# Performance work log

Measured on AMD Instinct MI355X. Metric: run time of the kernel, lower is better.

The kernel has to match this reference:

```python
import jax, jax.numpy as jnp
import numpy as np
from jax import lax

LN_EPS = 1e-5          # F.layer_norm default eps
W_EPS = 1e-7           # eps in ste_weights
Q_EPS = 1e-5           # BitLinear.eps used in activation clamp
Q_RANGE = 128          # 2**(num_bits-1), num_bits=8
DIM_IN = 2048
DIM_OUT = 8192
N_TOKENS = 8192


def setup_inputs() -> dict:
    key = jax.random.key(0)
    k1, k2 = jax.random.split(key)
    x = jax.random.normal(k1, (N_TOKENS, DIM_IN), dtype=jnp.float32)
    # nn.Linear default init: U(-1/sqrt(fan_in), 1/sqrt(fan_in))
    bound = 1.0 / np.sqrt(DIM_IN)
    weight = jax.random.uniform(k2, (DIM_OUT, DIM_IN), dtype=jnp.float32,
                                minval=-bound, maxval=bound)
    return {"x": x, "weight": weight}


def _bitlinear(x, weight):
    # layer_norm over feature dim, no affine params
    mu = jnp.mean(x, axis=-1, keepdims=True)
    var = jnp.mean(jnp.square(x - mu), axis=-1, keepdims=True)
    normed = (x - mu) * lax.rsqrt(var + LN_EPS)

    # scalars come from .item() in torch -> detached constants
    input_gamma = lax.stop_gradient(jnp.max(jnp.abs(normed)))
    w_gamma = lax.stop_gradient(jnp.mean(jnp.abs(weight)))

    # ternarize weights with straight-through estimator
    w_bin_ng = jnp.clip(jnp.round(weight / (w_gamma + W_EPS)), -1.0, 1.0)
    w_bin = weight + lax.stop_gradient(w_bin_ng - weight)

    # quantize activations to int8 range (kept in float, as in the source)
    q_in = jnp.clip(normed * (Q_RANGE / input_gamma),
                    -Q_RANGE + Q_EPS, Q_RANGE - Q_EPS)

    out = q_in @ w_bin.T  # [N, dim_out]; bias=False since mult_bias=False
    return out * (input_gamma * w_gamma / Q_RANGE)


def reference(x, weight):
    proj = _bitlinear(x, weight)               # [N, DIM_OUT]
    h, gate = jnp.split(proj, 2, axis=-1)      # chunk(2, dim=-1)
    return h * jax.nn.silu(gate)               # mult_bias == 1.0
```

## Files before the change

kernel.cpp:

```cpp
#include <hip/hip_runtime.h>
#include <hip/hip_bf16.h>
#include <cstdint>


#define N_TOK   8192
#define DIMIN   2048
#define DIMOUT  8192
#define NOUT    4096
#define W_ELEMS 16777216.0f
#define NPART   1024

typedef _Float16 f16x8 __attribute__((ext_vector_type(8)));
typedef _Float16 f16x4 __attribute__((ext_vector_type(4)));
typedef float    f32x4 __attribute__((ext_vector_type(4)));

__global__ __launch_bounds__(256) void ln_wsum_k(
    const float* __restrict__ x, const float* __restrict__ w,
    _Float16* __restrict__ qA, float* __restrict__ wpart) {
    const int b = blockIdx.x;
    const int t = threadIdx.x;
    if (b < N_TOK) {
        __shared__ float sh[8];
        const float4* xr = (const float4*)(x + (size_t)b * DIMIN);
        float4 a = xr[2 * t];
        float4 c = xr[2 * t + 1];
        float s = (a.x + a.y) + (a.z + a.w) + ((c.x + c.y) + (c.z + c.w));
#pragma unroll
        for (int o = 32; o > 0; o >>= 1) s += __shfl_down(s, o, 64);
        if ((t & 63) == 0) sh[t >> 6] = s;
        __syncthreads();
        const float mu = (sh[0] + sh[1] + sh[2] + sh[3]) * (1.0f / DIMIN);

        float d0 = a.x - mu, d1 = a.y - mu, d2 = a.z - mu, d3 = a.w - mu;
        float d4 = c.x - mu, d5 = c.y - mu, d6 = c.z - mu, d7 = c.w - mu;
        float ss = d0*d0 + d1*d1 + d2*d2 + d3*d3 + d4*d4 + d5*d5 + d6*d6 + d7*d7;
#pragma unroll
        for (int o = 32; o > 0; o >>= 1) ss += __shfl_down(ss, o, 64);
        if ((t & 63) == 0) sh[4 + (t >> 6)] = ss;
        __syncthreads();
        const float var = (sh[4] + sh[5] + sh[6] + sh[7]) * (1.0f / DIMIN);
        const float r = rsqrtf(var + 1e-5f);
        f16x8 o;
        o[0] = (_Float16)(d0 * r); o[1] = (_Float16)(d1 * r);
        o[2] = (_Float16)(d2 * r); o[3] = (_Float16)(d3 * r);
        o[4] = (_Float16)(d4 * r); o[5] = (_Float16)(d5 * r);
        o[6] = (_Float16)(d6 * r); o[7] = (_Float16)(d7 * r);
        ((f16x8*)(qA + (size_t)b * DIMIN))[t] = o;
    } else {
        const int p = b - N_TOK;
        float acc = 0.0f;
        const float4* w4 = (const float4*)w;
        for (unsigned i = (unsigned)p * 256u + t; i < 4194304u; i += 262144u) {
            float4 v = w4[i];
            acc += (fabsf(v.x) + fabsf(v.y)) + (fabsf(v.z) + fabsf(v.w));
        }
        __shared__ float shw[4];
#pragma unroll
        for (int o = 32; o > 0; o >>= 1) acc += __shfl_down(acc, o, 64);
        if ((t & 63) == 0) shw[t >> 6] = acc;
        __syncthreads();
        if (t == 0) wpart[p] = (shw[0] + shw[1]) + (shw[2] + shw[3]);
    }
}

__global__ __launch_bounds__(256) void ternW_k(
    const float* __restrict__ w, const float* __restrict__ wpart,
    float* __restrict__ sc, _Float16* __restrict__ q) {
    const int t = threadIdx.x;
    __shared__ float sh[4];
    float4 p = ((const float4*)wpart)[t];
    float acc = (p.x + p.y) + (p.z + p.w);
#pragma unroll
    for (int o = 32; o > 0; o >>= 1) acc += __shfl_down(acc, o, 64);
    if ((t & 63) == 0) sh[t >> 6] = acc;
    __syncthreads();
    const float wg = ((sh[0] + sh[1]) + (sh[2] + sh[3])) * (1.0f / W_ELEMS);
    if (blockIdx.x == 0 && t == 0) sc[0] = wg;
    const float invw = 1.0f / (wg + 1e-7f);
    for (unsigned i = blockIdx.x * 256u + t; i < 4194304u; i += 262144u) {
        float4 v = ((const float4*)w)[i];
        f16x4 o;
        o.x = (_Float16)fminf(fmaxf(rintf(v.x * invw), -1.0f), 1.0f);
        o.y = (_Float16)fminf(fmaxf(rintf(v.y * invw), -1.0f), 1.0f);
        o.z = (_Float16)fminf(fmaxf(rintf(v.z * invw), -1.0f), 1.0f);
        o.w = (_Float16)fminf(fmaxf(rintf(v.w * invw), -1.0f), 1.0f);
        ((f16x4*)q)[i] = o;
    }
}

__device__ __forceinline__ void ld16(const _Float16* g, _Float16* l) {
    __builtin_amdgcn_global_load_lds(
        (const __attribute__((address_space(1))) unsigned int*)g,
        (__attribute__((address_space(3))) unsigned int*)l, 16, 0, 0);
}


#define BAR    __builtin_amdgcn_s_barrier()
#define LGKM0  asm volatile("s_waitcnt lgkmcnt(0)" ::: "memory")
#define VMC(n) asm volatile("s_waitcnt vmcnt(" #n ")" ::: "memory")
#define PRIO1  __builtin_amdgcn_s_setprio(1)
#define PRIO0  __builtin_amdgcn_s_setprio(0)

#define MFMA16(ACC)                                                       \
    _Pragma("unroll") for (int mi = 0; mi < 4; ++mi)                      \
    _Pragma("unroll") for (int ni = 0; ni < 4; ++ni)                      \
        ACC[mi][ni] = __builtin_amdgcn_mfma_f32_16x16x32_f16(             \
            a[mi], b[ni], ACC[mi][ni], 0, 0, 0);

#define DS_AB(AOFF, BOFF_)                                                \
    _Pragma("unroll") for (int i = 0; i < 4; ++i) {                       \
        a[i] = *(const f16x8*)(Ac + (AOFF) + (i << 10));                  \
        b[i] = *(const f16x8*)(Bc + (BOFF_) + (i << 10));                 \
    }

#define DS_B(BOFF_)                                                       \
    _Pragma("unroll") for (int i = 0; i < 4; ++i)                         \
        b[i] = *(const f16x8*)(Bc + (BOFF_) + (i << 10));

__global__ __launch_bounds__(512, 2) void gemm_glu_k(
    const _Float16* __restrict__ Aq, const _Float16* __restrict__ Wq,
    const float* __restrict__ sc, float* __restrict__ out) {

    __shared__ __align__(16) _Float16 sm[65536];

    const int tid  = threadIdx.x;
    const int wave = tid >> 6;
    const int lane = tid & 63;

    const int swz = ((blockIdx.x & 7) << 7) + (blockIdx.x >> 3);
    const int m0 = (swz >> 5) << 8;
    const int n0 = (swz & 31) << 7;

    const int rs = (wave << 3) + (lane >> 3);
    const int kc = (((lane & 7) ^ ((lane >> 3) & 7)) << 3);
    const _Float16* pa = Aq + (size_t)(m0 + rs) * DIMIN + kc;
    const _Float16* pb = Wq + (size_t)(n0 + rs) * DIMIN + kc;

    const int fr   = lane & 15;
    const int quad = lane >> 4;
    const int xr   = fr & 7;
    const int wm = (wave >> 1) << 6;
    const int wn = (wave & 1) << 6;
    const int a0off = (wm + fr) * 64 + ((quad ^ xr) << 3);
    const int a1off = (wm + fr) * 64 + (((quad + 4) ^ xr) << 3);
    const int b0off = (wn + fr) * 64 + ((quad ^ xr) << 3);
    const int b1off = (wn + fr) * 64 + (((quad + 4) ^ xr) << 3);

    const float s = sc[0];

    f32x4 z = {0.0f, 0.0f, 0.0f, 0.0f};
    f32x4 acc_h[4][4], acc_g[4][4];
#pragma unroll
    for (int i = 0; i < 4; ++i)
#pragma unroll
        for (int j = 0; j < 4; ++j) { acc_h[i][j] = z; acc_g[i][j] = z; }

    {
        _Float16* dA = sm + (wave << 9);
        _Float16* dB = dA + 32768;
        ld16(pb,           dB);
        ld16(pb + 131072,  dB + 4096);
        ld16(pa,           dA);
        ld16(pa + 131072,  dA + 4096);
        ld16(pa + 262144,  dA + 8192);
        ld16(pa + 393216,  dA + 12288);
        ld16(pb + 8388608, dB + 8192);
        ld16(pb + 8519680, dB + 12288);
        pa += 64; pb += 64;
    }
    VMC(2);
    BAR;

    f16x8 a[4], b[4];
    for (int t = 0; t < 31; ++t) {
        const _Float16* Ac = sm + ((t & 1) << 14);
        const _Float16* Bc = Ac + 32768;
        _Float16* dA = sm + (((t + 1) & 1) << 14) + (wave << 9);
        _Float16* dB = dA + 32768;

        DS_AB(a0off, b0off);
        ld16(pb,          dB);
        ld16(pb + 131072, dB + 4096);
        BAR; LGKM0;
        PRIO1; MFMA16(acc_h); PRIO0;
        VMC(2);
        BAR;

        DS_B(8192 + b0off);
        ld16(pa,          dA);
        ld16(pa + 131072, dA + 4096);
        BAR; LGKM0;
        PRIO1; MFMA16(acc_g); PRIO0;
        BAR;

        DS_AB(a1off, b1off);
        ld16(pa + 262144, dA + 8192);
        ld16(pa + 393216, dA + 12288);
        BAR; LGKM0;
        PRIO1; MFMA16(acc_h); PRIO0;
        BAR;

        DS_B(8192 + b1off);
        ld16(pb + 8388608, dB + 8192);
        ld16(pb + 8519680, dB + 12288);
        BAR; LGKM0;
        PRIO1; MFMA16(acc_g); PRIO0;
        VMC(2);
        BAR;

        pa += 64; pb += 64;
    }

    {
        const _Float16* Ac = sm + 16384;
        const _Float16* Bc = Ac + 32768;

        DS_AB(a0off, b0off);
        BAR; LGKM0;
        PRIO1; MFMA16(acc_h); PRIO0;
        VMC(0);
        BAR;

        DS_B(8192 + b0off);
        BAR; LGKM0;
        PRIO1; MFMA16(acc_g); PRIO0;
        BAR;

        DS_AB(a1off, b1off);
        BAR; LGKM0;
        PRIO1; MFMA16(acc_h); PRIO0;
        BAR;

        DS_B(8192 + b1off);
        BAR; LGKM0;
        PRIO1; MFMA16(acc_g); PRIO0;
    }

    const int er = quad << 2;
#pragma unroll
    for (int mi = 0; mi < 4; ++mi)
#pragma unroll
        for (int ni = 0; ni < 4; ++ni)
#pragma unroll
            for (int r = 0; r < 4; ++r) {
                const int m = m0 + wm + (mi << 4) + er + r;
                const int n = n0 + wn + (ni << 4) + fr;
                const float h = acc_h[mi][ni][r] * s;
                const float g = acc_g[mi][ni][r] * s;
                out[(size_t)m * NOUT + n] = h * g / (1.0f + __expf(-g));
            }
}

extern "C" void kernel_launch(void* const* d_in, const int* in_sizes, int n_in,
                              void* d_out, int out_size, void* d_ws, size_t ws_size,
                              hipStream_t stream) {
    const float* x = (const float*)d_in[0];
    const float* w = (const float*)d_in[1];
    float* out = (float*)d_out;

    char* ws = (char*)d_ws;
    float* sc    = (float*)ws;
    float* wpart = (float*)(ws + 4096);
    _Float16* qA = (_Float16*)(ws + 16384);
    _Float16* wB = (_Float16*)(ws + 16384 + 33554432);

    ln_wsum_k<<<N_TOK + NPART, 256, 0, stream>>>(x, w, qA, wpart);
    ternW_k<<<NPART, 256, 0, stream>>>(w, wpart, sc, wB);

    gemm_glu_k<<<dim3(1024), dim3(512), 0, stream>>>(qA, wB, sc, out);
}
```

Before: 450.5 us.

## Use wave-per-row layernorm and keep both A fragments in registers in GEMM

The layernorm kernel now handles one row per wavefront (four rows per block) and reduces with xor shuffles, removing LDS reductions and block barriers. In the GEMM main loop, both A k-halves are held in separate register arrays, so the h and g accumulators reuse them and A is read from LDS once per tile instead of twice. The phase order and vmcnt waits are reworked to match the new LDS read and load schedule. This costs extra VGPRs under the 512-thread, 2-blocks-per-CU launch bound, which could cause spills or lower occupancy.

```diff
diff --git a/kernel.cpp b/kernel.cpp
--- a/kernel.cpp
+++ b/kernel.cpp
@@ -9,6 +9,7 @@
 #define NOUT    4096
 #define W_ELEMS 16777216.0f
 #define NPART   1024
+#define NLNB    2048
 
 typedef _Float16 f16x8 __attribute__((ext_vector_type(8)));
 typedef _Float16 f16x4 __attribute__((ext_vector_type(4)));
@@ -19,35 +20,49 @@
     _Float16* __restrict__ qA, float* __restrict__ wpart) {
     const int b = blockIdx.x;
     const int t = threadIdx.x;
-    if (b < N_TOK) {
-        __shared__ float sh[8];
-        const float4* xr = (const float4*)(x + (size_t)b * DIMIN);
-        float4 a = xr[2 * t];
-        float4 c = xr[2 * t + 1];
-        float s = (a.x + a.y) + (a.z + a.w) + ((c.x + c.y) + (c.z + c.w));
-#pragma unroll
-        for (int o = 32; o > 0; o >>= 1) s += __shfl_down(s, o, 64);
-        if ((t & 63) == 0) sh[t >> 6] = s;
-        __syncthreads();
-        const float mu = (sh[0] + sh[1] + sh[2] + sh[3]) * (1.0f / DIMIN);
-
-        float d0 = a.x - mu, d1 = a.y - mu, d2 = a.z - mu, d3 = a.w - mu;
-        float d4 = c.x - mu, d5 = c.y - mu, d6 = c.z - mu, d7 = c.w - mu;
-        float ss = d0*d0 + d1*d1 + d2*d2 + d3*d3 + d4*d4 + d5*d5 + d6*d6 + d7*d7;
-#pragma unroll
-        for (int o = 32; o > 0; o >>= 1) ss += __shfl_down(ss, o, 64);
-        if ((t & 63) == 0) sh[4 + (t >> 6)] = ss;
-        __syncthreads();
-        const float var = (sh[4] + sh[5] + sh[6] + sh[7]) * (1.0f / DIMIN);
+    if (b < NLNB) {
+        const int wv  = t >> 6;
+        const int ln  = t & 63;
+        const int row = (b << 2) + wv;
+        const float4* xr = (const float4*)(x + (size_t)row * DIMIN);
+        float4 v[8];
+#pragma unroll
+        for (int j = 0; j < 4; ++j) {
+            v[2 * j]     = xr[2 * ln + 128 * j];
+            v[2 * j + 1] = xr[2 * ln + 128 * j + 1];
+        }
+        float s = 0.0f;
+#pragma unroll
+        for (int j = 0; j < 8; ++j) s += (v[j].x + v[j].y) + (v[j].z + v[j].w);
+#pragma unroll
+        for (int o = 32; o > 0; o >>= 1) s += __shfl_xor(s, o, 64);
+        const float mu = s * (1.0f / DIMIN);
+
+        float ss = 0.0f;
+#pragma unroll
+        for (int j = 0; j < 8; ++j) {
+            float d0 = v[j].x - mu, d1 = v[j].y - mu;
+            float d2 = v[j].z - mu, d3 = v[j].w - mu;
+            ss += (d0 * d0 + d1 * d1) + (d2 * d2 + d3 * d3);
+        }
+#pragma unroll
+        for (int o = 32; o > 0; o >>= 1) ss += __shfl_xor(ss, o, 64);
+        const float var = ss * (1.0f / DIMIN);
         const float r = rsqrtf(var + 1e-5f);
-        f16x8 o;
-        o[0] = (_Float16)(d0 * r); o[1] = (_Float16)(d1 * r);
-        o[2] = (_Float16)(d2 * r); o[3] = (_Float16)(d3 * r);
-        o[4] = (_Float16)(d4 * r); o[5] = (_Float16)(d5 * r);
-        o[6] = (_Float16)(d6 * r); o[7] = (_Float16)(d7 * r);
-        ((f16x8*)(qA + (size_t)b * DIMIN))[t] = o;
+
+        f16x8* qr = (f16x8*)(qA + (size_t)row * DIMIN);
+#pragma unroll
+        for (int j = 0; j < 4; ++j) {
+            const float4 u0 = v[2 * j], u1 = v[2 * j + 1];
+            f16x8 o;
+            o[0] = (_Float16)((u0.x - mu) * r); o[1] = (_Float16)((u0.y - mu) * r);
+            o[2] = (_Float16)((u0.z - mu) * r); o[3] = (_Float16)((u0.w - mu) * r);
+            o[4] = (_Float16)((u1.x - mu) * r); o[5] = (_Float16)((u1.y - mu) * r);
+            o[6] = (_Float16)((u1.z - mu) * r); o[7] = (_Float16)((u1.w - mu) * r);
+            qr[ln + 64 * j] = o;
+        }
     } else {
-        const int p = b - N_TOK;
+        const int p = b - NLNB;
         float acc = 0.0f;
         const float4* w4 = (const float4*)w;
         for (unsigned i = (unsigned)p * 256u + t; i < 4194304u; i += 262144u) {
@@ -101,19 +116,17 @@
 #define PRIO1  __builtin_amdgcn_s_setprio(1)
 #define PRIO0  __builtin_amdgcn_s_setprio(0)
 
-#define MFMA16(ACC)                                                       \
+#define MFMA16(AARR, ACC)                                                 \
     _Pragma("unroll") for (int mi = 0; mi < 4; ++mi)                      \
     _Pragma("unroll") for (int ni = 0; ni < 4; ++ni)                      \
         ACC[mi][ni] = __builtin_amdgcn_mfma_f32_16x16x32_f16(             \
-            a[mi], b[ni], ACC[mi][ni], 0, 0, 0);
-
-#define DS_AB(AOFF, BOFF_)                                                \
-    _Pragma("unroll") for (int i = 0; i < 4; ++i) {                       \
-        a[i] = *(const f16x8*)(Ac + (AOFF) + (i << 10));                  \
-        b[i] = *(const f16x8*)(Bc + (BOFF_) + (i << 10));                 \
-    }
-
-#define DS_B(BOFF_)                                                       \
+            AARR[mi], b[ni], ACC[mi][ni], 0, 0, 0);
+
+#define DSA(AARR, AOFF)                                                   \
+    _Pragma("unroll") for (int i = 0; i < 4; ++i)                         \
+        AARR[i] = *(const f16x8*)(Ac + (AOFF) + (i << 10));
+
+#define DSB(BOFF_)                                                        \
     _Pragma("unroll") for (int i = 0; i < 4; ++i)                         \
         b[i] = *(const f16x8*)(Bc + (BOFF_) + (i << 10));
 
@@ -171,40 +184,40 @@
     VMC(2);
     BAR;
 
-    f16x8 a[4], b[4];
+    f16x8 a0[4], a1[4], b[4];
     for (int t = 0; t < 31; ++t) {
         const _Float16* Ac = sm + ((t & 1) << 14);
         const _Float16* Bc = Ac + 32768;
         _Float16* dA = sm + (((t + 1) & 1) << 14) + (wave << 9);
         _Float16* dB = dA + 32768;
 
-        DS_AB(a0off, b0off);
+        DSA(a0, a0off); DSB(b0off);
         ld16(pb,          dB);
         ld16(pb + 131072, dB + 4096);
         BAR; LGKM0;
-        PRIO1; MFMA16(acc_h); PRIO0;
-        VMC(2);
-        BAR;
-
-        DS_B(8192 + b0off);
+        PRIO1; MFMA16(a0, acc_h); PRIO0;
+        BAR;
+
+        DSA(a1, a1off); DSB(b1off);
         ld16(pa,          dA);
         ld16(pa + 131072, dA + 4096);
         BAR; LGKM0;
-        PRIO1; MFMA16(acc_g); PRIO0;
-        BAR;
-
-        DS_AB(a1off, b1off);
+        PRIO1; MFMA16(a1, acc_h); PRIO0;
+        VMC(4);
+        BAR;
+
+        DSB(8192 + b0off);
         ld16(pa + 262144, dA + 8192);
         ld16(pa + 393216, dA + 12288);
         BAR; LGKM0;
-        PRIO1; MFMA16(acc_h); PRIO0;
-        BAR;
-
-        DS_B(8192 + b1off);
+        PRIO1; MFMA16(a0, acc_g); PRIO0;
+        BAR;
+
+        DSB(8192 + b1off);
         ld16(pb + 8388608, dB + 8192);
         ld16(pb + 8519680, dB + 12288);
         BAR; LGKM0;
-        PRIO1; MFMA16(acc_g); PRIO0;
+        PRIO1; MFMA16(a1, acc_g); PRIO0;
         VMC(2);
         BAR;
 
@@ -215,25 +228,25 @@
         const _Float16* Ac = sm + 16384;
         const _Float16* Bc = Ac + 32768;
 
-        DS_AB(a0off, b0off);
-        BAR; LGKM0;
-        PRIO1; MFMA16(acc_h); PRIO0;
+        DSA(a0, a0off); DSB(b0off);
+        BAR; LGKM0;
+        PRIO1; MFMA16(a0, acc_h); PRIO0;
+        BAR;
+
+        DSA(a1, a1off); DSB(b1off);
+        BAR; LGKM0;
+        PRIO1; MFMA16(a1, acc_h); PRIO0;
         VMC(0);
         BAR;
 
-        DS_B(8192 + b0off);
-        BAR; LGKM0;
-        PRIO1; MFMA16(acc_g); PRIO0;
-        BAR;
-
-        DS_AB(a1off, b1off);
-        BAR; LGKM0;
-        PRIO1; MFMA16(acc_h); PRIO0;
-        BAR;
-
-        DS_B(8192 + b1off);
-        BAR; LGKM0;
-        PRIO1; MFMA16(acc_g); PRIO0;
+        DSB(8192 + b0off);
+        BAR; LGKM0;
+        PRIO1; MFMA16(a0, acc_g); PRIO0;
+        BAR;
+
+        DSB(8192 + b1off);
+        BAR; LGKM0;
+        PRIO1; MFMA16(a1, acc_g); PRIO0;
     }
 
     const int er = quad << 2;
@@ -264,7 +277,7 @@
     _Float16* qA = (_Float16*)(ws + 16384);
     _Float16* wB = (_Float16*)(ws + 16384 + 33554432);
 
-    ln_wsum_k<<<N_TOK + NPART, 256, 0, stream>>>(x, w, qA, wpart);
+    ln_wsum_k<<<NLNB + NPART, 256, 0, stream>>>(x, w, qA, wpart);
     ternW_k<<<NPART, 256, 0, stream>>>(w, wpart, sc, wB);
 
     gemm_glu_k<<<dim3(1024), dim3(512), 0, stream>>>(qA, wB, sc, out);
```

Result: no change. 447.7 us (-0.6%).
